# Optimization experiments

Measured on AMD Instinct MI355X. Metric: run time of the kernel, lower is better.

The kernel has to match this reference:

```python
import jax, jax.numpy as jnp
import numpy as np

N = 20000   # nodes
E = 320000  # directed edges (before self-loops)
D = 64      # input_dim
H = 10      # GAT heads
HD = H * D  # 640
NEG_SLOPE = 0.2


def setup_inputs() -> dict:
    key = jax.random.key(0)
    ks = jax.random.split(key, 10)
    return {
        "x": jax.random.normal(ks[0], (N, D), jnp.float32),
        "W_gat": jax.random.normal(ks[1], (D, HD), jnp.float32) / np.sqrt(D).astype(np.float32),
        "att_src": jax.random.normal(ks[2], (H, D), jnp.float32) / np.sqrt(D).astype(np.float32),
        "att_dst": jax.random.normal(ks[3], (H, D), jnp.float32) / np.sqrt(D).astype(np.float32),
        "b_gat": jnp.zeros((HD,), jnp.float32),
        "W_gcn": jax.random.normal(ks[4], (HD, HD), jnp.float32) / np.sqrt(HD).astype(np.float32),
        "b_gcn": jnp.zeros((HD,), jnp.float32),
        "W1": jax.random.normal(ks[5], (2 * HD, 1500), jnp.float32) / np.sqrt(2 * HD).astype(np.float32),
        "b1": jnp.zeros((1500,), jnp.float32),
        "W2": jax.random.normal(ks[6], (1500, 10), jnp.float32) / np.sqrt(1500).astype(np.float32),
        "b2": jnp.zeros((10,), jnp.float32),
        "edge_index": jax.random.randint(ks[7], (2, E), 0, N, dtype=jnp.int64),
    }


def _forward(x, W_gat, att_src, att_dst, b_gat, W_gcn, b_gcn, W1, b1, W2, b2, edge_index):
    n = x.shape[0]
    # add self-loops (PyG default for both GATConv and GCNConv)
    loop = jnp.arange(n, dtype=edge_index.dtype)
    ei = jnp.concatenate([edge_index, jnp.stack([loop, loop])], axis=1)
    src, dst = ei[0], ei[1]

    # ---- GATConv(D -> D, heads=H, concat) ----
    xl = (x @ W_gat).reshape(n, H, D)                      # [N,H,D]
    a_src = jnp.einsum('nhd,hd->nh', xl, att_src)          # [N,H]
    a_dst = jnp.einsum('nhd,hd->nh', xl, att_dst)          # [N,H]
    alpha = jax.nn.leaky_relu(a_src[src] + a_dst[dst], NEG_SLOPE)  # [E',H]
    m = jax.ops.segment_max(alpha, dst, num_segments=n)    # segment softmax over incoming edges
    ex = jnp.exp(alpha - m[dst])
    den = jax.ops.segment_sum(ex, dst, num_segments=n)
    w = ex / (den[dst] + 1e-16)                            # [E',H]
    msg = xl[src] * w[:, :, None]                          # [E',H,D]
    x1 = jax.ops.segment_sum(msg, dst, num_segments=n).reshape(n, HD) + b_gat
    x1 = jax.nn.relu(x1)

    # ---- GCNConv(HD -> HD), symmetric norm with self-loops ----
    deg = jax.ops.segment_sum(jnp.ones(ei.shape[1], x.dtype), dst, num_segments=n)
    dinv = jnp.where(deg > 0, jax.lax.rsqrt(deg), 0.0)
    norm = dinv[src] * dinv[dst]                           # [E']
    xw = x1 @ W_gcn                                        # [N,HD]
    x2 = jax.ops.segment_sum(xw[src] * norm[:, None], dst, num_segments=n) + b_gcn
    x2 = jax.nn.relu(x2)

    # ---- global max/mean pool (batch=None -> single graph) + MLP head ----
    pooled = jnp.concatenate([x2.max(axis=0, keepdims=True),
                              x2.mean(axis=0, keepdims=True)], axis=1)  # [1, 2*HD]
    h = jax.nn.relu(pooled @ W1 + b1)
    # dropout is identity in eval mode
    return h @ W2 + b2                                     # [1, 10]


def reference(x, W_gat, att_src, att_dst, b_gat, W_gcn, b_gcn, W1, b1, W2, b2, edge_index):
    return _forward(x, W_gat, att_src, att_dst, b_gat, W_gcn, b_gcn, W1, b1, W2, b2, edge_index)
```

## Files before the change

kernel.cpp:

```cpp
#include <hip/hip_runtime.h>
#include <hip/hip_bf16.h>
#include <math.h>

#define NN 20000
#define DD 64
#define HH 10
#define HDIM 640
#define NEG 0.2f
#define H1 1500
#define ASTRIDE 12
#define BKK 128

typedef _Float16 half8 __attribute__((ext_vector_type(8)));
typedef _Float16 half4v __attribute__((ext_vector_type(4)));
typedef _Float16 half2v __attribute__((ext_vector_type(2)));
typedef float f32x4 __attribute__((ext_vector_type(4)));

__global__ __launch_bounds__(256) void k_cvtB(const float* __restrict__ Wgcn,
                                              const float* __restrict__ Wg,
                                              _Float16* __restrict__ Wbt,
                                              _Float16* __restrict__ WgT)
{
    __shared__ float t[32][33];
    const int bx = blockIdx.x;
    int by = blockIdx.y;
    const float* W; _Float16* WT; int rows, cols;
    if (by < 20) { W = Wgcn; WT = Wbt; rows = HDIM; cols = HDIM; }
    else         { W = Wg;   WT = WgT; rows = DD;   cols = HDIM; by -= 20; }
    const int lx = threadIdx.x & 31, ly = threadIdx.x >> 5;
    #pragma unroll
    for (int i = ly; i < 32; i += 8)
        t[i][lx] = W[(size_t)(by * 32 + i) * cols + bx * 32 + lx];
    __syncthreads();
    #pragma unroll
    for (int j = ly; j < 32; j += 8)
        WT[(size_t)(bx * 32 + j) * rows + by * 32 + lx] = (_Float16)t[lx][j];
}

__global__ __launch_bounds__(256) void k_gemm1(
    const float* __restrict__ x, const _Float16* __restrict__ WgT,
    const float* __restrict__ att_s, const float* __restrict__ att_d,
    _Float16* __restrict__ xl, float* __restrict__ a_src, float* __restrict__ a_dst)
{
    __shared__ _Float16 As[128][72];
    __shared__ _Float16 Bs[64][72];
    const int tid = threadIdx.x;
    const int m0 = blockIdx.x * 128;
    const int h  = blockIdx.y;
    const int n0 = h * 64;

    {
        const int row = tid >> 1, ch = (tid & 1) * 32;
        const int gr = m0 + row;
        if (gr < NN) {
            const float* xp = &x[(size_t)gr * DD + ch];
            #pragma unroll
            for (int i = 0; i < 8; ++i) {
                const float4 v = *(const float4*)&xp[i * 4];
                half4v o = {(_Float16)v.x, (_Float16)v.y, (_Float16)v.z, (_Float16)v.w};
                *(half4v*)&As[row][ch + i * 4] = o;
            }
        } else {
            const half8 z = {0, 0, 0, 0, 0, 0, 0, 0};
            #pragma unroll
            for (int i = 0; i < 4; ++i) *(half8*)&As[row][ch + i * 8] = z;
        }
    }
    {
        const int row = tid >> 2, part = (tid & 3) * 16;
        const _Float16* wp = &WgT[(size_t)(n0 + row) * DD + part];
        *(half8*)&Bs[row][part]     = *(const half8*)&wp[0];
        *(half8*)&Bs[row][part + 8] = *(const half8*)&wp[8];
    }
    __syncthreads();

    const int lane = tid & 63, wave = tid >> 6;
    const int l15 = lane & 15, quad = lane >> 4;
    f32x4 acc[2][4];
    #pragma unroll
    for (int r = 0; r < 2; ++r)
        #pragma unroll
        for (int c = 0; c < 4; ++c) acc[r][c] = (f32x4){0.f, 0.f, 0.f, 0.f};

    #pragma unroll
    for (int ks = 0; ks < 2; ++ks) {
        const half8 a0 = *(const half8*)&As[wave * 32 + l15][ks * 32 + quad * 8];
        const half8 a1 = *(const half8*)&As[wave * 32 + 16 + l15][ks * 32 + quad * 8];
        #pragma unroll
        for (int c = 0; c < 4; ++c) {
            const half8 b = *(const half8*)&Bs[c * 16 + l15][ks * 32 + quad * 8];
            acc[0][c] = __builtin_amdgcn_mfma_f32_16x16x32_f16(a0, b, acc[0][c], 0, 0, 0);
            acc[1][c] = __builtin_amdgcn_mfma_f32_16x16x32_f16(a1, b, acc[1][c], 0, 0, 0);
        }
    }

    float asv[4], adv[4];
    #pragma unroll
    for (int c = 0; c < 4; ++c) {
        asv[c] = att_s[h * DD + c * 16 + l15];
        adv[c] = att_d[h * DD + c * 16 + l15];
    }
    #pragma unroll
    for (int r = 0; r < 2; ++r) {
        float ps[4] = {0.f, 0.f, 0.f, 0.f}, pd[4] = {0.f, 0.f, 0.f, 0.f};
        #pragma unroll
        for (int c = 0; c < 4; ++c)
            #pragma unroll
            for (int g = 0; g < 4; ++g) {
                ps[g] = fmaf(acc[r][c][g], asv[c], ps[g]);
                pd[g] = fmaf(acc[r][c][g], adv[c], pd[g]);
            }
        #pragma unroll
        for (int m = 1; m <= 8; m <<= 1)
            #pragma unroll
            for (int g = 0; g < 4; ++g) {
                ps[g] += __shfl_xor(ps[g], m);
                pd[g] += __shfl_xor(pd[g], m);
            }
        #pragma unroll
        for (int c = 0; c < 4; ++c)
            #pragma unroll
            for (int g = 0; g < 4; ++g) {
                const int row = m0 + wave * 32 + r * 16 + quad * 4 + g;
                if (row < NN)
                    xl[(size_t)row * HDIM + n0 + c * 16 + l15] = (_Float16)acc[r][c][g];
            }
        if (l15 == 0)
            #pragma unroll
            for (int g = 0; g < 4; ++g) {
                const int row = m0 + wave * 32 + r * 16 + quad * 4 + g;
                if (row < NN) {
                    a_src[(size_t)row * ASTRIDE + h] = ps[g];
                    a_dst[(size_t)row * ASTRIDE + h] = pd[g];
                }
            }
    }
}

__global__ void k_count(const int* __restrict__ ei, int E, int* __restrict__ cnt)
{
    const int e = blockIdx.x * blockDim.x + threadIdx.x;
    if (e >= E + NN) return;
    const int d = (e < E) ? ei[E + e] : (e - E);
    atomicAdd(&cnt[d], 1);
}

__global__ __launch_bounds__(1024) void k_scan(const int* __restrict__ cnt,
                                               int* __restrict__ rowptr,
                                               float* __restrict__ dinv)
{
    __shared__ int sh[1024];
    const int t = threadIdx.x;
    const int CH = 20;
    const int base = t * CH;
    int loc[CH];
    int s = 0;
    #pragma unroll
    for (int i = 0; i < CH; ++i) {
        const int idx = base + i;
        const int c = (idx < NN) ? cnt[idx] : 0;
        loc[i] = s; s += c;
    }
    sh[t] = s; __syncthreads();
    for (int off = 1; off < 1024; off <<= 1) {
        const int v = (t >= off) ? sh[t - off] : 0;
        __syncthreads();
        sh[t] += v;
        __syncthreads();
    }
    const int prev = (t == 0) ? 0 : sh[t - 1];
    #pragma unroll
    for (int i = 0; i < CH; ++i) {
        const int idx = base + i;
        if (idx < NN) {
            rowptr[idx] = prev + loc[i];
            dinv[idx]   = rsqrtf((float)cnt[idx]);
        }
    }
    if (t == 1023) rowptr[NN] = sh[1023];
}

__global__ void k_fill(const int* __restrict__ ei, int E,
                       const int* __restrict__ rowptr,
                       int* __restrict__ cursor, int* __restrict__ csr,
                       const float* __restrict__ dinv, float* __restrict__ wn,
                       const float* __restrict__ aS, const float* __restrict__ aD,
                       float* __restrict__ wgat)
{
    const int e = blockIdx.x * blockDim.x + threadIdx.x;
    if (e >= E + NN) return;
    int s, d;
    if (e < E) { s = ei[e]; d = ei[E + e]; } else { s = d = e - E; }
    const int pos = atomicAdd(&cursor[d], 1);
    const int idx = rowptr[d] + pos;
    csr[idx] = s;
    wn[idx]  = dinv[s] * dinv[d];

    const f32x4 s0 = *(const f32x4*)&aS[(size_t)s * ASTRIDE];
    const f32x4 s1 = *(const f32x4*)&aS[(size_t)s * ASTRIDE + 4];
    const float2 s2 = *(const float2*)&aS[(size_t)s * ASTRIDE + 8];
    const f32x4 d0 = *(const f32x4*)&aD[(size_t)d * ASTRIDE];
    const f32x4 d1 = *(const f32x4*)&aD[(size_t)d * ASTRIDE + 4];
    const float2 d2 = *(const float2*)&aD[(size_t)d * ASTRIDE + 8];
    const float av[10] = {s0.x + d0.x, s0.y + d0.y, s0.z + d0.z, s0.w + d0.w,
                          s1.x + d1.x, s1.y + d1.y, s1.z + d1.z, s1.w + d1.w,
                          s2.x + d2.x, s2.y + d2.y};
    float* wp = &wgat[(size_t)idx * HH];
    #pragma unroll
    for (int h = 0; h < 10; ++h) {
        float a = av[h];
        a = (a >= 0.f) ? a : NEG * a;
        wp[h] = __expf(a);
    }
}

__global__ __launch_bounds__(256) void k_gat_gather(
    const int* __restrict__ rowptr, const int* __restrict__ csr,
    const float* __restrict__ wgat, const _Float16* __restrict__ xl,
    const float* __restrict__ b_gat, _Float16* __restrict__ x1)
{
    const int wave = threadIdx.x >> 6, lane = threadIdx.x & 63;
    const int n = blockIdx.x * 4 + wave;
    const int c0 = lane * 8;
    const int h0 = lane >> 3;
    const bool dual = (lane < 16);
    const int c1 = 512 + lane * 8;
    const int h1 = 8 + (lane >> 3);

    float acc0[8], acc1[8], ws0 = 0.f, ws1 = 0.f;
    #pragma unroll
    for (int i = 0; i < 8; ++i) { acc0[i] = 0.f; acc1[i] = 0.f; }

    const int j0 = rowptr[n], j1 = rowptr[n + 1];
    int j = j0;
    for (; j + 3 < j1; j += 4) {
        const int sA = csr[j], sB = csr[j + 1], sC = csr[j + 2], sD = csr[j + 3];
        const float wA0 = wgat[(size_t)(j + 0) * HH + h0];
        const float wB0 = wgat[(size_t)(j + 1) * HH + h0];
        const float wC0 = wgat[(size_t)(j + 2) * HH + h0];
        const float wD0 = wgat[(size_t)(j + 3) * HH + h0];
        ws0 += wA0 + wB0 + wC0 + wD0;
        const half8 vA0 = *(const half8*)&xl[(size_t)sA * HDIM + c0];
        const half8 vB0 = *(const half8*)&xl[(size_t)sB * HDIM + c0];
        const half8 vC0 = *(const half8*)&xl[(size_t)sC * HDIM + c0];
        const half8 vD0 = *(const half8*)&xl[(size_t)sD * HDIM + c0];
        #pragma unroll
        for (int i = 0; i < 8; ++i) {
            acc0[i] = fmaf(wA0, (float)vA0[i], acc0[i]);
            acc0[i] = fmaf(wB0, (float)vB0[i], acc0[i]);
            acc0[i] = fmaf(wC0, (float)vC0[i], acc0[i]);
            acc0[i] = fmaf(wD0, (float)vD0[i], acc0[i]);
        }
        if (dual) {
            const float wA1 = wgat[(size_t)(j + 0) * HH + h1];
            const float wB1 = wgat[(size_t)(j + 1) * HH + h1];
            const float wC1 = wgat[(size_t)(j + 2) * HH + h1];
            const float wD1 = wgat[(size_t)(j + 3) * HH + h1];
            ws1 += wA1 + wB1 + wC1 + wD1;
            const half8 vA1 = *(const half8*)&xl[(size_t)sA * HDIM + c1];
            const half8 vB1 = *(const half8*)&xl[(size_t)sB * HDIM + c1];
            const half8 vC1 = *(const half8*)&xl[(size_t)sC * HDIM + c1];
            const half8 vD1 = *(const half8*)&xl[(size_t)sD * HDIM + c1];
            #pragma unroll
            for (int i = 0; i < 8; ++i) {
                acc1[i] = fmaf(wA1, (float)vA1[i], acc1[i]);
                acc1[i] = fmaf(wB1, (float)vB1[i], acc1[i]);
                acc1[i] = fmaf(wC1, (float)vC1[i], acc1[i]);
                acc1[i] = fmaf(wD1, (float)vD1[i], acc1[i]);
            }
        }
    }
    for (; j < j1; ++j) {
        const int sA = csr[j];
        const float wA0 = wgat[(size_t)j * HH + h0];
        ws0 += wA0;
        const half8 vA0 = *(const half8*)&xl[(size_t)sA * HDIM + c0];
        #pragma unroll
        for (int i = 0; i < 8; ++i) acc0[i] = fmaf(wA0, (float)vA0[i], acc0[i]);
        if (dual) {
            const float wA1 = wgat[(size_t)j * HH + h1];
            ws1 += wA1;
            const half8 vA1 = *(const half8*)&xl[(size_t)sA * HDIM + c1];
            #pragma unroll
            for (int i = 0; i < 8; ++i) acc1[i] = fmaf(wA1, (float)vA1[i], acc1[i]);
        }
    }

    {
        const float rr = 1.f / (ws0 + 1e-16f);
        const float4 ba = *(const float4*)&b_gat[c0];
        const float4 bb = *(const float4*)&b_gat[c0 + 4];
        const float bv[8] = {ba.x, ba.y, ba.z, ba.w, bb.x, bb.y, bb.z, bb.w};
        half8 o;
        #pragma unroll
        for (int i = 0; i < 8; ++i) {
            const float v = fmaf(acc0[i], rr, bv[i]);
            o[i] = (_Float16)((v > 0.f) ? v : 0.f);
        }
        *(half8*)&x1[(size_t)n * HDIM + c0] = o;
    }
    if (dual) {
        const float rr = 1.f / (ws1 + 1e-16f);
        const float4 ba = *(const float4*)&b_gat[c1];
        const float4 bb = *(const float4*)&b_gat[c1 + 4];
        const float bv[8] = {ba.x, ba.y, ba.z, ba.w, bb.x, bb.y, bb.z, bb.w};
        half8 o;
        #pragma unroll
        for (int i = 0; i < 8; ++i) {
            const float v = fmaf(acc1[i], rr, bv[i]);
            o[i] = (_Float16)((v > 0.f) ? v : 0.f);
        }
        *(half8*)&x1[(size_t)n * HDIM + c1] = o;
    }
}

__global__ __launch_bounds__(256) void k_gemm2(const _Float16* __restrict__ X,
                                               const _Float16* __restrict__ Wbt,
                                               _Float16* __restrict__ Y)
{
    __shared__ _Float16 Bs[128 * BKK];
    const int tid = threadIdx.x;
    const int lane = tid & 63, wave = tid >> 6;
    const int l15 = lane & 15, quad = lane >> 4;
    const int m0 = blockIdx.x * 128 + wave * 32;
    const int n0 = blockIdx.y * 128;
    const int l7 = l15 & 7;

    f32x4 acc[2][8];
    #pragma unroll
    for (int r = 0; r < 2; ++r)
        #pragma unroll
        for (int c = 0; c < 8; ++c) acc[r][c] = (f32x4){0.f, 0.f, 0.f, 0.f};

    const int jrow = lane >> 4;
    const int jchunk = lane & 15;

    const _Float16* a0p = &X[(size_t)(m0 + l15) * HDIM + quad * 8];
    const _Float16* a1p = a0p + (size_t)16 * HDIM;

    for (int kb = 0; kb < HDIM; kb += BKK) {
        #pragma unroll
        for (int i = 0; i < 8; ++i) {
            const int r = (wave * 8 + i) * 4 + jrow;
            const int ck = jchunk ^ (r & 7);
            const _Float16* src = &Wbt[(size_t)(n0 + r) * HDIM + kb + ck * 8];
            __builtin_amdgcn_global_load_lds(
                (const __attribute__((address_space(1))) void*)src,
                (__attribute__((address_space(3))) void*)&Bs[(size_t)(wave * 8 + i) * 512],
                16, 0, 0);
        }
        half8 a0[4], a1[4];
        #pragma unroll
        for (int ks = 0; ks < 4; ++ks) {
            a0[ks] = *(const half8*)(a0p + kb + ks * 32);
            a1[ks] = *(const half8*)(a1p + kb + ks * 32);
        }
        __syncthreads();
        #pragma unroll
        for (int ks = 0; ks < 4; ++ks) {
            #pragma unroll
            for (int c = 0; c < 8; ++c) {
                const int br = c * 16 + l15;
                const int ck = (4 * ks + quad) ^ l7;
                const half8 b = *(const half8*)&Bs[(size_t)br * BKK + ck * 8];
                acc[0][c] = __builtin_amdgcn_mfma_f32_16x16x32_f16(a0[ks], b, acc[0][c], 0, 0, 0);
                acc[1][c] = __builtin_amdgcn_mfma_f32_16x16x32_f16(a1[ks], b, acc[1][c], 0, 0, 0);
            }
        }
        __syncthreads();
    }

    #pragma unroll
    for (int r = 0; r < 2; ++r) {
        #pragma unroll
        for (int c = 0; c < 8; ++c) {
            #pragma unroll
            for (int g = 0; g < 4; ++g) {
                const int row = m0 + r * 16 + quad * 4 + g;
                if (row < NN)
                    Y[(size_t)row * HDIM + n0 + c * 16 + l15] = (_Float16)acc[r][c][g];
            }
        }
    }
}

__global__ __launch_bounds__(256) void k_gcn_gather(
    const int* __restrict__ rowptr, const int* __restrict__ csr,
    const float* __restrict__ wn, const _Float16* __restrict__ xw,
    const float* __restrict__ b_gcn, _Float16* __restrict__ x2)
{
    const int wave = threadIdx.x >> 6, lane = threadIdx.x & 63;
    const int n = blockIdx.x * 4 + wave;
    const int c0 = lane * 8;
    const bool dual = (lane < 16);
    const int c1 = 512 + lane * 8;

    float acc0[8], acc1[8];
    #pragma unroll
    for (int i = 0; i < 8; ++i) { acc0[i] = 0.f; acc1[i] = 0.f; }

    const int j0 = rowptr[n], j1 = rowptr[n + 1];
    int j = j0;
    for (; j + 3 < j1; j += 4) {
        const int sA = csr[j], sB = csr[j + 1], sC = csr[j + 2], sD = csr[j + 3];
        const float wA = wn[j], wB = wn[j + 1], wC = wn[j + 2], wD = wn[j + 3];
        const half8 vA0 = *(const half8*)&xw[(size_t)sA * HDIM + c0];
        const half8 vB0 = *(const half8*)&xw[(size_t)sB * HDIM + c0];
        const half8 vC0 = *(const half8*)&xw[(size_t)sC * HDIM + c0];
        const half8 vD0 = *(const half8*)&xw[(size_t)sD * HDIM + c0];
        #pragma unroll
        for (int i = 0; i < 8; ++i) {
            acc0[i] = fmaf(wA, (float)vA0[i], acc0[i]);
            acc0[i] = fmaf(wB, (float)vB0[i], acc0[i]);
            acc0[i] = fmaf(wC, (float)vC0[i], acc0[i]);
            acc0[i] = fmaf(wD, (float)vD0[i], acc0[i]);
        }
        if (dual) {
            const half8 vA1 = *(const half8*)&xw[(size_t)sA * HDIM + c1];
            const half8 vB1 = *(const half8*)&xw[(size_t)sB * HDIM + c1];
            const half8 vC1 = *(const half8*)&xw[(size_t)sC * HDIM + c1];
            const half8 vD1 = *(const half8*)&xw[(size_t)sD * HDIM + c1];
            #pragma unroll
            for (int i = 0; i < 8; ++i) {
                acc1[i] = fmaf(wA, (float)vA1[i], acc1[i]);
                acc1[i] = fmaf(wB, (float)vB1[i], acc1[i]);
                acc1[i] = fmaf(wC, (float)vC1[i], acc1[i]);
                acc1[i] = fmaf(wD, (float)vD1[i], acc1[i]);
            }
        }
    }
    for (; j < j1; ++j) {
        const int sA = csr[j];
        const float wA = wn[j];
        const half8 vA0 = *(const half8*)&xw[(size_t)sA * HDIM + c0];
        #pragma unroll
        for (int i = 0; i < 8; ++i) acc0[i] = fmaf(wA, (float)vA0[i], acc0[i]);
        if (dual) {
            const half8 vA1 = *(const half8*)&xw[(size_t)sA * HDIM + c1];
            #pragma unroll
            for (int i = 0; i < 8; ++i) acc1[i] = fmaf(wA, (float)vA1[i], acc1[i]);
        }
    }

    {
        const float4 ba = *(const float4*)&b_gcn[c0];
        const float4 bb = *(const float4*)&b_gcn[c0 + 4];
        const float bv[8] = {ba.x, ba.y, ba.z, ba.w, bb.x, bb.y, bb.z, bb.w};
        half8 o;
        #pragma unroll
        for (int i = 0; i < 8; ++i) {
            const float v = acc0[i] + bv[i];
            o[i] = (_Float16)((v > 0.f) ? v : 0.f);
        }
        *(half8*)&x2[(size_t)n * HDIM + c0] = o;
    }
    if (dual) {
        const float4 ba = *(const float4*)&b_gcn[c1];
        const float4 bb = *(const float4*)&b_gcn[c1 + 4];
        const float bv[8] = {ba.x, ba.y, ba.z, ba.w, bb.x, bb.y, bb.z, bb.w};
        half8 o;
        #pragma unroll
        for (int i = 0; i < 8; ++i) {
            const float v = acc1[i] + bv[i];
            o[i] = (_Float16)((v > 0.f) ? v : 0.f);
        }
        *(half8*)&x2[(size_t)n * HDIM + c1] = o;
    }
}

__global__ __launch_bounds__(64) void k_pool(const _Float16* __restrict__ x2,
                                             float* __restrict__ pmax,
                                             float* __restrict__ psum)
{
    const int t = threadIdx.x;
    const int col = blockIdx.x * 128 + t * 2;
    const int nb = blockIdx.y;
    float mx0 = 0.f, mx1 = 0.f, s0 = 0.f, s1 = 0.f;
    const int nend = nb * 250 + 250;
    for (int n = nb * 250; n < nend; ++n) {
        const half2v v = *(const half2v*)&x2[(size_t)n * HDIM + col];
        const float v0 = (float)v.x, v1 = (float)v.y;
        mx0 = fmaxf(mx0, v0); mx1 = fmaxf(mx1, v1);
        s0 += v0; s1 += v1;
    }
    atomicMax((int*)&pmax[col],     __float_as_int(mx0));
    atomicMax((int*)&pmax[col + 1], __float_as_int(mx1));
    atomicAdd(&psum[col],     s0);
    atomicAdd(&psum[col + 1], s1);
}

__global__ __launch_bounds__(256) void k_mlp1(const float* __restrict__ pmax,
                                              const float* __restrict__ psum,
                                              const float* __restrict__ W1,
                                              float* __restrict__ hacc)
{
    __shared__ float pl[80];
    const int t = threadIdx.x;
    const int i0 = blockIdx.y * 80;
    if (t < 80) {
        const int i = i0 + t;
        pl[t] = (i < HDIM) ? pmax[i] : psum[i - HDIM] * (1.0f / NN);
    }
    __syncthreads();
    const int j = blockIdx.x * 256 + t;
    if (j >= H1) return;
    float acc = 0.f;
    #pragma unroll 8
    for (int i = 0; i < 80; ++i)
        acc = fmaf(pl[i], W1[(size_t)(i0 + i) * H1 + j], acc);
    atomicAdd(&hacc[j], acc);
}

__global__ __launch_bounds__(256) void k_mlp2(const float* __restrict__ hacc,
                                              const float* __restrict__ b1,
                                              const float* __restrict__ W2,
                                              const float* __restrict__ b2,
                                              float* __restrict__ out)
{
    __shared__ float hsh[H1];
    __shared__ float red[256];
    const int t = threadIdx.x;
    for (int i = t; i < H1; i += 256) {
        const float v = hacc[i] + b1[i];
        hsh[i] = (v > 0.f) ? v : 0.f;
    }
    __syncthreads();
    float acc[10];
    #pragma unroll
    for (int k = 0; k < 10; ++k) acc[k] = 0.f;
    for (int i = t; i < H1; i += 256) {
        const float h = hsh[i];
        #pragma unroll
        for (int k = 0; k < 10; ++k) acc[k] = fmaf(h, W2[i * 10 + k], acc[k]);
    }
    for (int k = 0; k < 10; ++k) {
        red[t] = acc[k]; __syncthreads();
        for (int s2 = 128; s2 > 0; s2 >>= 1) {
            if (t < s2) red[t] += red[t + s2];
            __syncthreads();
        }
        if (t == 0) out[k] = red[0] + b2[k];
        __syncthreads();
    }
}

extern "C" void kernel_launch(void* const* d_in, const int* in_sizes, int n_in,
                              void* d_out, int out_size, void* d_ws, size_t ws_size,
                              hipStream_t stream)
{
    const float* x     = (const float*)d_in[0];
    const float* Wg    = (const float*)d_in[1];
    const float* att_s = (const float*)d_in[2];
    const float* att_d = (const float*)d_in[3];
    const float* b_gat = (const float*)d_in[4];
    const float* Wgcn  = (const float*)d_in[5];
    const float* b_gcn = (const float*)d_in[6];
    const float* W1    = (const float*)d_in[7];
    const float* b1    = (const float*)d_in[8];
    const float* W2    = (const float*)d_in[9];
    const float* b2    = (const float*)d_in[10];
    const int*   ei    = (const int*)d_in[11];
    const int E = in_sizes[11] / 2;
    const int EP = E + NN;
    float* out = (float*)d_out;

    char* wsp = (char*)d_ws;
    size_t off = 0;
    auto alc = [&](size_t b) { void* p = wsp + off; off += (b + 255) & ~(size_t)255; return p; };
    _Float16* bufA = (_Float16*)alc((size_t)NN * HDIM * 2);
    _Float16* bufB = (_Float16*)alc((size_t)NN * HDIM * 2);
    float* aS     = (float*)alc((size_t)NN * ASTRIDE * 4);
    float* aD     = (float*)alc((size_t)NN * ASTRIDE * 4);
    int*   rowptr = (int*)alc((size_t)(NN + 1) * 4);
    int*   csr    = (int*)alc((size_t)EP * 4);
    float* dinv   = (float*)alc((size_t)NN * 4);
    float* wn     = (float*)alc((size_t)EP * 4);
    float* wgat   = (float*)alc((size_t)EP * HH * 4);
    _Float16* Wbt = (_Float16*)alc((size_t)HDIM * HDIM * 2);
    _Float16* WgT = (_Float16*)alc((size_t)HDIM * DD * 2);
    const size_t zoff = off;
    int*   cnt    = (int*)alc((size_t)NN * 4);
    int*   cursor = (int*)alc((size_t)NN * 4);
    float* pmax   = (float*)alc((size_t)HDIM * 4);
    float* psum   = (float*)alc((size_t)HDIM * 4);
    float* hacc   = (float*)alc((size_t)H1 * 4);
    const size_t zsize = off - zoff;

    hipMemsetAsync(cnt, 0, zsize, stream);

    dim3 gw(HDIM / 32, HDIM / 32 + DD / 32);
    k_cvtB<<<gw, 256, 0, stream>>>(Wgcn, Wg, Wbt, WgT);
    dim3 g1((NN + 127) / 128, HH);
    k_gemm1<<<g1, 256, 0, stream>>>(x, WgT, att_s, att_d, bufA, aS, aD);
    k_count<<<(EP + 255) / 256, 256, 0, stream>>>(ei, E, cnt);
    k_scan<<<1, 1024, 0, stream>>>(cnt, rowptr, dinv);
    k_fill<<<(EP + 255) / 256, 256, 0, stream>>>(ei, E, rowptr, cursor, csr,
                                                 dinv, wn, aS, aD, wgat);
    k_gat_gather<<<NN / 4, 256, 0, stream>>>(rowptr, csr, wgat, bufA, b_gat, bufB);
    dim3 g2((NN + 127) / 128, HDIM / 128);
    k_gemm2<<<g2, 256, 0, stream>>>(bufB, Wbt, bufA);
    k_gcn_gather<<<NN / 4, 256, 0, stream>>>(rowptr, csr, wn, bufA, b_gcn, bufB);
    dim3 gp(HDIM / 128, 80);
    k_pool<<<gp, 64, 0, stream>>>(bufB, pmax, psum);
    dim3 gm1(6, 16);
    k_mlp1<<<gm1, 256, 0, stream>>>(pmax, psum, W1, hacc);
    k_mlp2<<<1, 256, 0, stream>>>(hacc, b1, W2, b2, out);
}
```

Measured before the change: 380.3 us.

## Aggregate before GCN GEMM and fuse bias, ReLU and pooling into GEMM epilogue

Uses linearity of GCN aggregation to reorder it, so the sparse gather runs on x1 before the dense GEMM: (A·x1)·W instead of A·(x1·W). The GEMM epilogue then adds the bias, applies ReLU and reduces column max and sum through shared-memory atomics followed by global atomics. This drops the separate pooling kernel and the write and re-read of the x2 activation. The intermediate aggregate is rounded to fp16 before the GEMM, which changes rounding order slightly, and the global atomics now come from every GEMM tile.

```diff
diff --git a/kernel.cpp b/kernel.cpp
--- a/kernel.cpp
+++ b/kernel.cpp
@@ -314,9 +314,83 @@
     }
 }
 
+__global__ __launch_bounds__(256) void k_gcn_gather(
+    const int* __restrict__ rowptr, const int* __restrict__ csr,
+    const float* __restrict__ wn, const _Float16* __restrict__ x1,
+    _Float16* __restrict__ t)
+{
+    const int wave = threadIdx.x >> 6, lane = threadIdx.x & 63;
+    const int n = blockIdx.x * 4 + wave;
+    const int c0 = lane * 8;
+    const bool dual = (lane < 16);
+    const int c1 = 512 + lane * 8;
+
+    float acc0[8], acc1[8];
+    #pragma unroll
+    for (int i = 0; i < 8; ++i) { acc0[i] = 0.f; acc1[i] = 0.f; }
+
+    const int j0 = rowptr[n], j1 = rowptr[n + 1];
+    int j = j0;
+    for (; j + 3 < j1; j += 4) {
+        const int sA = csr[j], sB = csr[j + 1], sC = csr[j + 2], sD = csr[j + 3];
+        const float wA = wn[j], wB = wn[j + 1], wC = wn[j + 2], wD = wn[j + 3];
+        const half8 vA0 = *(const half8*)&x1[(size_t)sA * HDIM + c0];
+        const half8 vB0 = *(const half8*)&x1[(size_t)sB * HDIM + c0];
+        const half8 vC0 = *(const half8*)&x1[(size_t)sC * HDIM + c0];
+        const half8 vD0 = *(const half8*)&x1[(size_t)sD * HDIM + c0];
+        #pragma unroll
+        for (int i = 0; i < 8; ++i) {
+            acc0[i] = fmaf(wA, (float)vA0[i], acc0[i]);
+            acc0[i] = fmaf(wB, (float)vB0[i], acc0[i]);
+            acc0[i] = fmaf(wC, (float)vC0[i], acc0[i]);
+            acc0[i] = fmaf(wD, (float)vD0[i], acc0[i]);
+        }
+        if (dual) {
+            const half8 vA1 = *(const half8*)&x1[(size_t)sA * HDIM + c1];
+            const half8 vB1 = *(const half8*)&x1[(size_t)sB * HDIM + c1];
+            const half8 vC1 = *(const half8*)&x1[(size_t)sC * HDIM + c1];
+            const half8 vD1 = *(const half8*)&x1[(size_t)sD * HDIM + c1];
+            #pragma unroll
+            for (int i = 0; i < 8; ++i) {
+                acc1[i] = fmaf(wA, (float)vA1[i], acc1[i]);
+                acc1[i] = fmaf(wB, (float)vB1[i], acc1[i]);
+                acc1[i] = fmaf(wC, (float)vC1[i], acc1[i]);
+                acc1[i] = fmaf(wD, (float)vD1[i], acc1[i]);
+            }
+        }
+    }
+    for (; j < j1; ++j) {
+        const int sA = csr[j];
+        const float wA = wn[j];
+        const half8 vA0 = *(const half8*)&x1[(size_t)sA * HDIM + c0];
+        #pragma unroll
+        for (int i = 0; i < 8; ++i) acc0[i] = fmaf(wA, (float)vA0[i], acc0[i]);
+        if (dual) {
+            const half8 vA1 = *(const half8*)&x1[(size_t)sA * HDIM + c1];
+            #pragma unroll
+            for (int i = 0; i < 8; ++i) acc1[i] = fmaf(wA, (float)vA1[i], acc1[i]);
+        }
+    }
+
+    {
+        half8 o;
+        #pragma unroll
+        for (int i = 0; i < 8; ++i) o[i] = (_Float16)acc0[i];
+        *(half8*)&t[(size_t)n * HDIM + c0] = o;
+    }
+    if (dual) {
+        half8 o;
+        #pragma unroll
+        for (int i = 0; i < 8; ++i) o[i] = (_Float16)acc1[i];
+        *(half8*)&t[(size_t)n * HDIM + c1] = o;
+    }
+}
+
 __global__ __launch_bounds__(256) void k_gemm2(const _Float16* __restrict__ X,
                                                const _Float16* __restrict__ Wbt,
-                                               _Float16* __restrict__ Y)
+                                               const float* __restrict__ b_gcn,
+                                               float* __restrict__ pmax,
+                                               float* __restrict__ psum)
 {
     __shared__ _Float16 Bs[128 * BKK];
     const int tid = threadIdx.x;
@@ -370,123 +444,40 @@
         __syncthreads();
     }
 
-    #pragma unroll
-    for (int r = 0; r < 2; ++r) {
-        #pragma unroll
-        for (int c = 0; c < 8; ++c) {
+    float lmax[8], lsum[8];
+    #pragma unroll
+    for (int c = 0; c < 8; ++c) { lmax[c] = 0.f; lsum[c] = 0.f; }
+    #pragma unroll
+    for (int c = 0; c < 8; ++c) {
+        const float bb = b_gcn[n0 + c * 16 + l15];
+        #pragma unroll
+        for (int r = 0; r < 2; ++r)
             #pragma unroll
             for (int g = 0; g < 4; ++g) {
                 const int row = m0 + r * 16 + quad * 4 + g;
-                if (row < NN)
-                    Y[(size_t)row * HDIM + n0 + c * 16 + l15] = (_Float16)acc[r][c][g];
-            }
-        }
-    }
-}
-
-__global__ __launch_bounds__(256) void k_gcn_gather(
-    const int* __restrict__ rowptr, const int* __restrict__ csr,
-    const float* __restrict__ wn, const _Float16* __restrict__ xw,
-    const float* __restrict__ b_gcn, _Float16* __restrict__ x2)
-{
-    const int wave = threadIdx.x >> 6, lane = threadIdx.x & 63;
-    const int n = blockIdx.x * 4 + wave;
-    const int c0 = lane * 8;
-    const bool dual = (lane < 16);
-    const int c1 = 512 + lane * 8;
-
-    float acc0[8], acc1[8];
-    #pragma unroll
-    for (int i = 0; i < 8; ++i) { acc0[i] = 0.f; acc1[i] = 0.f; }
-
-    const int j0 = rowptr[n], j1 = rowptr[n + 1];
-    int j = j0;
-    for (; j + 3 < j1; j += 4) {
-        const int sA = csr[j], sB = csr[j + 1], sC = csr[j + 2], sD = csr[j + 3];
-        const float wA = wn[j], wB = wn[j + 1], wC = wn[j + 2], wD = wn[j + 3];
-        const half8 vA0 = *(const half8*)&xw[(size_t)sA * HDIM + c0];
-        const half8 vB0 = *(const half8*)&xw[(size_t)sB * HDIM + c0];
-        const half8 vC0 = *(const half8*)&xw[(size_t)sC * HDIM + c0];
-        const half8 vD0 = *(const half8*)&xw[(size_t)sD * HDIM + c0];
-        #pragma unroll
-        for (int i = 0; i < 8; ++i) {
-            acc0[i] = fmaf(wA, (float)vA0[i], acc0[i]);
-            acc0[i] = fmaf(wB, (float)vB0[i], acc0[i]);
-            acc0[i] = fmaf(wC, (float)vC0[i], acc0[i]);
-            acc0[i] = fmaf(wD, (float)vD0[i], acc0[i]);
-        }
-        if (dual) {
-            const half8 vA1 = *(const half8*)&xw[(size_t)sA * HDIM + c1];
-            const half8 vB1 = *(const half8*)&xw[(size_t)sB * HDIM + c1];
-            const half8 vC1 = *(const half8*)&xw[(size_t)sC * HDIM + c1];
-            const half8 vD1 = *(const half8*)&xw[(size_t)sD * HDIM + c1];
-            #pragma unroll
-            for (int i = 0; i < 8; ++i) {
-                acc1[i] = fmaf(wA, (float)vA1[i], acc1[i]);
-                acc1[i] = fmaf(wB, (float)vB1[i], acc1[i]);
-                acc1[i] = fmaf(wC, (float)vC1[i], acc1[i]);
-                acc1[i] = fmaf(wD, (float)vD1[i], acc1[i]);
-            }
-        }
-    }
-    for (; j < j1; ++j) {
-        const int sA = csr[j];
-        const float wA = wn[j];
-        const half8 vA0 = *(const half8*)&xw[(size_t)sA * HDIM + c0];
-        #pragma unroll
-        for (int i = 0; i < 8; ++i) acc0[i] = fmaf(wA, (float)vA0[i], acc0[i]);
-        if (dual) {
-            const half8 vA1 = *(const half8*)&xw[(size_t)sA * HDIM + c1];
-            #pragma unroll
-            for (int i = 0; i < 8; ++i) acc1[i] = fmaf(wA, (float)vA1[i], acc1[i]);
-        }
-    }
-
-    {
-        const float4 ba = *(const float4*)&b_gcn[c0];
-        const float4 bb = *(const float4*)&b_gcn[c0 + 4];
-        const float bv[8] = {ba.x, ba.y, ba.z, ba.w, bb.x, bb.y, bb.z, bb.w};
-        half8 o;
-        #pragma unroll
-        for (int i = 0; i < 8; ++i) {
-            const float v = acc0[i] + bv[i];
-            o[i] = (_Float16)((v > 0.f) ? v : 0.f);
-        }
-        *(half8*)&x2[(size_t)n * HDIM + c0] = o;
-    }
-    if (dual) {
-        const float4 ba = *(const float4*)&b_gcn[c1];
-        const float4 bb = *(const float4*)&b_gcn[c1 + 4];
-        const float bv[8] = {ba.x, ba.y, ba.z, ba.w, bb.x, bb.y, bb.z, bb.w};
-        half8 o;
-        #pragma unroll
-        for (int i = 0; i < 8; ++i) {
-            const float v = acc1[i] + bv[i];
-            o[i] = (_Float16)((v > 0.f) ? v : 0.f);
-        }
-        *(half8*)&x2[(size_t)n * HDIM + c1] = o;
-    }
-}
-
-__global__ __launch_bounds__(64) void k_pool(const _Float16* __restrict__ x2,
-                                             float* __restrict__ pmax,
-                                             float* __restrict__ psum)
-{
-    const int t = threadIdx.x;
-    const int col = blockIdx.x * 128 + t * 2;
-    const int nb = blockIdx.y;
-    float mx0 = 0.f, mx1 = 0.f, s0 = 0.f, s1 = 0.f;
-    const int nend = nb * 250 + 250;
-    for (int n = nb * 250; n < nend; ++n) {
-        const half2v v = *(const half2v*)&x2[(size_t)n * HDIM + col];
-        const float v0 = (float)v.x, v1 = (float)v.y;
-        mx0 = fmaxf(mx0, v0); mx1 = fmaxf(mx1, v1);
-        s0 += v0; s1 += v1;
-    }
-    atomicMax((int*)&pmax[col],     __float_as_int(mx0));
-    atomicMax((int*)&pmax[col + 1], __float_as_int(mx1));
-    atomicAdd(&psum[col],     s0);
-    atomicAdd(&psum[col + 1], s1);
+                if (row < NN) {
+                    float v = acc[r][c][g] + bb;
+                    v = (v > 0.f) ? v : 0.f;
+                    lmax[c] = fmaxf(lmax[c], v);
+                    lsum[c] += v;
+                }
+            }
+    }
+    float* redm = (float*)Bs;
+    float* reds = redm + 128;
+    if (tid < 128) { redm[tid] = 0.f; reds[tid] = 0.f; }
+    __syncthreads();
+    #pragma unroll
+    for (int c = 0; c < 8; ++c) {
+        const int col = c * 16 + l15;
+        atomicMax((int*)&redm[col], __float_as_int(lmax[c]));
+        atomicAdd(&reds[col], lsum[c]);
+    }
+    __syncthreads();
+    if (tid < 128) {
+        atomicMax((int*)&pmax[n0 + tid], __float_as_int(redm[tid]));
+        atomicAdd(&psum[n0 + tid], reds[tid]);
+    }
 }
 
 __global__ __launch_bounds__(256) void k_mlp1(const float* __restrict__ pmax,
@@ -597,11 +588,9 @@
     k_fill<<<(EP + 255) / 256, 256, 0, stream>>>(ei, E, rowptr, cursor, csr,
                                                  dinv, wn, aS, aD, wgat);
     k_gat_gather<<<NN / 4, 256, 0, stream>>>(rowptr, csr, wgat, bufA, b_gat, bufB);
+    k_gcn_gather<<<NN / 4, 256, 0, stream>>>(rowptr, csr, wn, bufB, bufA);
     dim3 g2((NN + 127) / 128, HDIM / 128);
-    k_gemm2<<<g2, 256, 0, stream>>>(bufB, Wbt, bufA);
-    k_gcn_gather<<<NN / 4, 256, 0, stream>>>(rowptr, csr, wn, bufA, b_gcn, bufB);
-    dim3 gp(HDIM / 128, 80);
-    k_pool<<<gp, 64, 0, stream>>>(bufB, pmax, psum);
+    k_gemm2<<<g2, 256, 0, stream>>>(bufA, Wbt, b_gcn, pmax, psum);
     dim3 gm1(6, 16);
     k_mlp1<<<gm1, 256, 0, stream>>>(pmax, psum, W1, hacc);
     k_mlp2<<<1, 256, 0, stream>>>(hacc, b1, W2, b2, out);
```

Result: faster. 367.3 us, median of 2 (-3.4%).
